# Kernel tuning notes

Measured on AMD Instinct MI355X. Metric: run time of the kernel, lower is better.

Reference implementation:

```python
import jax, jax.numpy as jnp
import numpy as np

N, E, V, H, HEADS, L, B = 20000, 320000, 100, 128, 3, 2, 200
NEG = 0.2   # leaky_relu negative_slope
EPS = 1e-5  # LayerNorm eps


def _mean_nodes(x, gid):
    # dgl.mean_nodes: per-graph mean of node features
    s = jax.ops.segment_sum(x, gid, num_segments=B)
    c = jax.ops.segment_sum(jnp.ones((x.shape[0], 1), x.dtype), gid, num_segments=B)
    return s / jnp.maximum(c, 1.0)


def _gat_layer(h, src, dst, Wn, bn, att, Ws, b, gamma, beta):
    # weight_node: Linear(H, H*HEADS)
    wv = (h @ Wn + bn).reshape(-1, HEADS, H)
    u = wv[src]  # [E, heads, H] gathered src features
    # attn = leaky_relu(sum(cat(u, v) * w_att)) split into u/v halves (no concat materialized)
    attn = (jnp.einsum('ehd,hd->eh', u, att[:, :H])
            + jnp.einsum('ehd,hd->eh', wv[dst], att[:, H:]))
    attn = jax.nn.leaky_relu(attn, NEG)  # [E, heads]
    # segment softmax over incoming edges of each dst node (mailbox softmax)
    m = jax.ops.segment_max(attn, dst, num_segments=N)
    m = jnp.where(jnp.isfinite(m), m, 0.0)
    e = jnp.exp(attn - m[dst])
    s = jax.ops.segment_sum(e, dst, num_segments=N)
    score = e / s[dst]
    agg = jax.ops.segment_sum(score[:, :, None] * u, dst, num_segments=N)  # [N, heads, H]
    res = agg.reshape(-1, HEADS * H) @ Ws + b
    # DGL leaves zero-in-degree nodes with zero reduced features (reduce_func never runs)
    has_in = jax.ops.segment_sum(jnp.ones((E,), h.dtype), dst, num_segments=N) > 0
    res = jnp.where(has_in[:, None], res, 0.0)
    x = res + h  # residual, then LayerNorm, relu (dropout is eval-mode identity)
    mu = jnp.mean(x, -1, keepdims=True)
    var = jnp.var(x, -1, keepdims=True)
    x = (x - mu) * jax.lax.rsqrt(var + EPS) * gamma + beta
    return jax.nn.relu(x)


def _gru_dir(x, Wih, Whh, bih, bhh, reverse):
    # torch nn.GRU single direction; x: [B, T, in]
    def step(hprev, xt):
        gi = xt @ Wih.T + bih
        gh = hprev @ Whh.T + bhh
        ir, iz, inn = jnp.split(gi, 3, -1)
        hr, hz, hn = jnp.split(gh, 3, -1)
        r = jax.nn.sigmoid(ir + hr)
        z = jax.nn.sigmoid(iz + hz)
        n = jnp.tanh(inn + r * hn)
        hnew = (1.0 - z) * n + z * hprev
        return hnew, hnew
    h0 = jnp.zeros((x.shape[0], Whh.shape[1]), x.dtype)
    hT, ys = jax.lax.scan(step, h0, jnp.swapaxes(x, 0, 1), reverse=reverse)
    return jnp.swapaxes(ys, 0, 1), hT


def setup_inputs() -> dict:
    key = jax.random.key(0)
    k = jax.random.split(key, 16)
    sc = 0.05
    return {
        'h': jax.random.normal(k[0], (N, H), jnp.float32),
        'wid': jax.random.randint(k[1], (N,), 0, V),
        'src': jax.random.randint(k[2], (E,), 0, N),
        'dst': jax.random.randint(k[3], (E,), 0, N),
        'graph_ids': jnp.sort(jax.random.randint(k[4], (N,), 0, B)),
        'proj_W': jax.random.normal(k[5], (V + H, H), jnp.float32) * sc,
        'proj_b': jnp.zeros((H,), jnp.float32),
        'conv_Wn': jax.random.normal(k[6], (L, H, HEADS * H), jnp.float32) * sc,
        'conv_bn': jnp.zeros((L, HEADS * H), jnp.float32),
        'conv_att': jax.random.normal(k[7], (L, HEADS, 2 * H), jnp.float32) * sc,
        'conv_Ws': jax.random.normal(k[8], (L, HEADS * H, H), jnp.float32) * sc,
        'conv_b': jnp.zeros((L, H), jnp.float32),
        'conv_gamma': jnp.ones((L, H), jnp.float32),
        'conv_beta': jnp.zeros((L, H), jnp.float32),
        'gru_Wih0': jax.random.normal(k[9], (2, 3 * H, H), jnp.float32) * sc,
        'gru_Whh0': jax.random.normal(k[10], (2, 3 * H, H), jnp.float32) * sc,
        'gru_bih0': jnp.zeros((2, 3 * H), jnp.float32),
        'gru_bhh0': jnp.zeros((2, 3 * H), jnp.float32),
        'gru_Wih1': jax.random.normal(k[11], (2, 3 * H, 2 * H), jnp.float32) * sc,
        'gru_Whh1': jax.random.normal(k[12], (2, 3 * H, H), jnp.float32) * sc,
        'gru_bih1': jnp.zeros((2, 3 * H), jnp.float32),
        'gru_bhh1': jnp.zeros((2, 3 * H), jnp.float32),
    }


def reference(h, wid, src, dst, graph_ids, proj_W, proj_b, conv_Wn, conv_bn, conv_att, conv_Ws, conv_b, conv_gamma, conv_beta, gru_Wih0, gru_Whh0, gru_bih0, gru_bhh0, gru_Wih1, gru_Whh1, gru_bih1, gru_bhh1):
    one_hot = jax.nn.one_hot(wid, V, dtype=h.dtype)
    hcur = jnp.concatenate([one_hot, h], -1) @ proj_W + proj_b  # project
    readouts = [_mean_nodes(hcur, graph_ids)]
    for l in range(L):
        hcur = _gat_layer(hcur, src, dst, conv_Wn[l], conv_bn[l], conv_att[l],
                          conv_Ws[l], conv_b[l], conv_gamma[l], conv_beta[l])
        readouts.append(_mean_nodes(hcur, graph_ids))
    x = jnp.stack(readouts, 1)  # [B, L+1, H] GRU readout sequence
    finals = []
    for (Wih, Whh, bih, bhh) in ((gru_Wih0, gru_Whh0, gru_bih0, gru_bhh0),
                                 (gru_Wih1, gru_Whh1, gru_bih1, gru_bhh1)):
        yf, hf = _gru_dir(x, Wih[0], Whh[0], bih[0], bhh[0], False)
        yb, hb = _gru_dir(x, Wih[1], Whh[1], bih[1], bhh[1], True)
        x = jnp.concatenate([yf, yb], -1)
        finals += [hf, hb]
    # torch returns h_n [num_layers*2, B, H]; module takes mean over dim 0
    return jnp.mean(jnp.stack(finals, 0), 0)  # [B, H]
```

## Files before the change

kernel.cpp:

```cpp
#include <hip/hip_runtime.h>
#include <cstddef>
#include <cstdint>

static constexpr int Nn    = 20000;
static constexpr int Ee    = 320000;
static constexpr int Vv    = 100;
static constexpr int Hh    = 128;
static constexpr int HEADS = 3;
static constexpr int Bb    = 200;
static constexpr float NEG = 0.2f;
static constexpr float EPS = 1e-5f;

typedef short bf16x8 __attribute__((ext_vector_type(8)));
typedef float f32x4  __attribute__((ext_vector_type(4)));

__device__ inline unsigned short bf16_rne(float x) {
    unsigned u = __builtin_bit_cast(unsigned, x);
    u += 0x7FFFu + ((u >> 16) & 1u);
    return (unsigned short)(u >> 16);
}
__device__ inline float bf16_f(unsigned short h) {
    unsigned u = ((unsigned)h) << 16;
    return __builtin_bit_cast(float, u);
}
__device__ inline float bf_lo(unsigned u) { return __builtin_bit_cast(float, u << 16); }
__device__ inline float bf_hi(unsigned u) { return __builtin_bit_cast(float, u & 0xFFFF0000u); }
__device__ inline float lrelu(float a) { return a >= 0.f ? a : NEG * a; }
__device__ inline float sigmoidf(float x) { return 1.f / (1.f + __expf(-x)); }

__global__ __launch_bounds__(1024) void scan_offsets(const int* __restrict__ deg,
                                                     int* __restrict__ offs,
                                                     int* __restrict__ cur) {
    __shared__ int sums[1024];
    const int tid = threadIdx.x;
    const int per = (Nn + 1023) >> 10;
    int begin = tid * per;
    int end = begin + per; if (end > Nn) end = Nn;
    if (begin > Nn) begin = Nn;
    int s = 0;
    for (int i = begin; i < end; i++) s += deg[i];
    sums[tid] = s;
    __syncthreads();
    for (int off = 1; off < 1024; off <<= 1) {
        int v = (tid >= off) ? sums[tid - off] : 0;
        __syncthreads();
        sums[tid] += v;
        __syncthreads();
    }
    int run = sums[tid] - s;
    for (int i = begin; i < end; i++) {
        offs[i] = run; cur[i] = run;
        run += deg[i];
    }
    if (end == Nn) offs[Nn] = run;
}

__global__ void fill_csr(const int* __restrict__ dst, const int* __restrict__ src,
                         int* __restrict__ cur, int* __restrict__ csrc) {
    for (int i = blockIdx.x * blockDim.x + threadIdx.x; i < Ee; i += gridDim.x * blockDim.x) {
        int p = atomicAdd(&cur[dst[i]], 1);
        csrc[p] = src[i];
    }
}

struct PrepArgs {
    const float *projW, *convWn, *convWs, *convAtt, *convBn, *convB;
    const float *Wih0, *Whh0, *Wih1, *Whh1;
    const int *gid, *dst;
    unsigned short *pBth, *pBtl;
    unsigned short *WfTh0, *WfTl0, *WfTh1, *WfTl1;
    float *vavd, *vc, *biasF;
    float *WihT0, *WhhT0, *WihT1, *WhhT1;
    int *goffs, *deg;
};

__device__ inline void wsplit(const float* B, int K, int N, int idx,
                              unsigned short* Bth, unsigned short* Btl) {
    int k = idx / N, n = idx - k * N;
    float v = B[idx];
    unsigned short h = bf16_rne(v);
    unsigned short l = bf16_rne(v - bf16_f(h));
    Bth[(size_t)n * K + k] = h;
    Btl[(size_t)n * K + k] = l;
}
__device__ inline void gruT(const float* W, int K, int idx, float* WT) {
    int d = idx / (384 * K);
    int r = idx - d * 384 * K;
    int j = r / K, k = r - j * K;
    WT[(size_t)d * K * 384 + (size_t)k * 384 + j] = W[idx];
}

__global__ void prep_all(PrepArgs a) {
    int i = blockIdx.x * blockDim.x + threadIdx.x;
    if (i < 16384) { wsplit(a.projW, 128, 128, i, a.pBth, a.pBtl); return; } i -= 16384;
#pragma unroll
    for (int l = 0; l < 2; l++) {
        if (i < 49152) {
            int k = i >> 7, c = i & 127;
            int h = k >> 7, i_ = k & 127;
            const float* wn = a.convWn + (size_t)l * 49152 + (size_t)i_ * 384 + h * 128;
            const float* ws = a.convWs + (size_t)l * 49152 + (size_t)(h * 128) * 128 + c;
            float v = 0.f;
            for (int j = 0; j < 128; j++) v += wn[j] * ws[(size_t)j * 128];
            unsigned short hi = bf16_rne(v);
            unsigned short lo = bf16_rne(v - bf16_f(hi));
            unsigned short* th = l ? a.WfTh1 : a.WfTh0;
            unsigned short* tl = l ? a.WfTl1 : a.WfTl0;
            th[(size_t)c * 384 + k] = hi;
            tl[(size_t)c * 384 + k] = lo;
            return;
        }
        i -= 49152;
    }
    if (i < 1536) {
        int l = i / 768, r = i % 768;
        int sd = r / 384, rr = r % 384, h = rr >> 7, i_ = rr & 127;
        const float* wn = a.convWn + (size_t)l * 49152 + (size_t)i_ * 384 + h * 128;
        const float* at = a.convAtt + l * 768 + h * 256 + sd * 128;
        float v = 0.f;
        for (int j = 0; j < 128; j++) v += wn[j] * at[j];
        a.vavd[i] = v;
        return;
    } i -= 1536;
    if (i < 12) {
        int l = i / 6, r = i % 6, sd = r / 3, h = r % 3;
        const float* bn = a.convBn + l * 384 + h * 128;
        const float* at = a.convAtt + l * 768 + h * 256 + sd * 128;
        float v = 0.f;
        for (int j = 0; j < 128; j++) v += bn[j] * at[j];
        a.vc[i] = v;
        return;
    } i -= 12;
    if (i < 256) {
        int l = i >> 7, c = i & 127;
        const float* bn = a.convBn + l * 384;
        const float* ws = a.convWs + (size_t)l * 49152 + c;
        float v = a.convB[l * 128 + c];
        for (int k = 0; k < 384; k++) v += bn[k] * ws[(size_t)k * 128];
        a.biasF[i] = v;
        return;
    } i -= 256;
    if (i < 98304)  { gruT(a.Wih0, 128, i, a.WihT0); return; }  i -= 98304;
    if (i < 98304)  { gruT(a.Whh0, 128, i, a.WhhT0); return; }  i -= 98304;
    if (i < 196608) { gruT(a.Wih1, 256, i, a.WihT1); return; }  i -= 196608;
    if (i < 98304)  { gruT(a.Whh1, 128, i, a.WhhT1); return; }  i -= 98304;
    if (i < Nn) {
        int g = a.gid[i];
        if (i == 0) { for (int b = 0; b <= g; b++) a.goffs[b] = 0; }
        else { int pg = a.gid[i - 1]; for (int b = pg + 1; b <= g; b++) a.goffs[b] = i; }
        if (i == Nn - 1) { for (int b = g + 1; b <= Bb; b++) a.goffs[b] = Nn; }
        return;
    } i -= Nn;
    if (i < Ee) atomicAdd(&a.deg[a.dst[i]], 1);
}

struct GArgs {
    const float* A; const unsigned short* Bth; const unsigned short* Btl;
    const float* bias; int M, K;
    const int* wid; const float* projW;
    const int* deg; const float* gamma; const float* beta;
    float* hcur;
    const int* gid; float* reado;
    const float* vavd; const float* vc;
    float* adf; float* addf;
    unsigned short* hb;
};

template <int MODE>
__global__ __launch_bounds__(256) void gemm_fused(GArgs a) {
    __shared__ unsigned short As_hi[32][40];
    __shared__ unsigned short As_lo[32][40];
    __shared__ unsigned short Bs_hi[128][40];
    __shared__ unsigned short Bs_lo[128][40];
    __shared__ float ytile[32][132];
    __shared__ float sred[6][32][4];
    __shared__ int sgid[32];
    const int tid  = threadIdx.x;
    const int row0 = blockIdx.y * 32;
    const int wn   = tid >> 6;
    const int L    = tid & 63;
    const int lrow = L & 15;
    const int lq   = L >> 4;
    const int K = a.K;

    f32x4 acc[2][2];
#pragma unroll
    for (int i = 0; i < 2; i++)
#pragma unroll
        for (int j = 0; j < 2; j++) acc[i][j] = (f32x4){0.f, 0.f, 0.f, 0.f};

    for (int kb = 0; kb < K; kb += 32) {
        {
            int m  = tid >> 3;
            int kq = (tid & 7) * 4;
            float4 v = *(const float4*)(a.A + (size_t)(row0 + m) * K + kb + kq);
            unsigned short h0 = bf16_rne(v.x), h1 = bf16_rne(v.y),
                           h2 = bf16_rne(v.z), h3 = bf16_rne(v.w);
            *(short4*)&As_hi[m][kq] = make_short4((short)h0, (short)h1, (short)h2, (short)h3);
            *(short4*)&As_lo[m][kq] = make_short4((short)bf16_rne(v.x - bf16_f(h0)),
                                                  (short)bf16_rne(v.y - bf16_f(h1)),
                                                  (short)bf16_rne(v.z - bf16_f(h2)),
                                                  (short)bf16_rne(v.w - bf16_f(h3)));
        }
        {
            int n  = tid >> 1;
            int kh = (tid & 1) * 16;
            const unsigned short* sh = a.Bth + (size_t)n * K + kb + kh;
            const unsigned short* sl = a.Btl + (size_t)n * K + kb + kh;
            *(float4*)&Bs_hi[n][kh]     = *(const float4*)sh;
            *(float4*)&Bs_hi[n][kh + 8] = *(const float4*)(sh + 8);
            *(float4*)&Bs_lo[n][kh]     = *(const float4*)sl;
            *(float4*)&Bs_lo[n][kh + 8] = *(const float4*)(sl + 8);
        }
        __syncthreads();
        bf16x8 ah[2], al[2], bh[2], bl[2];
#pragma unroll
        for (int mi = 0; mi < 2; mi++) {
            int r = mi * 16 + lrow;
            ah[mi] = *(const bf16x8*)&As_hi[r][lq * 8];
            al[mi] = *(const bf16x8*)&As_lo[r][lq * 8];
        }
#pragma unroll
        for (int ni = 0; ni < 2; ni++) {
            int r = wn * 32 + ni * 16 + lrow;
            bh[ni] = *(const bf16x8*)&Bs_hi[r][lq * 8];
            bl[ni] = *(const bf16x8*)&Bs_lo[r][lq * 8];
        }
#pragma unroll
        for (int mi = 0; mi < 2; mi++)
#pragma unroll
            for (int ni = 0; ni < 2; ni++) {
                acc[mi][ni] = __builtin_amdgcn_mfma_f32_16x16x32_bf16(ah[mi], bh[ni], acc[mi][ni], 0, 0, 0);
                acc[mi][ni] = __builtin_amdgcn_mfma_f32_16x16x32_bf16(ah[mi], bl[ni], acc[mi][ni], 0, 0, 0);
                acc[mi][ni] = __builtin_amdgcn_mfma_f32_16x16x32_bf16(al[mi], bh[ni], acc[mi][ni], 0, 0, 0);
            }
        __syncthreads();
    }

#pragma unroll
    for (int ni = 0; ni < 2; ni++) {
        float bb = a.bias[wn * 32 + ni * 16 + lrow];
#pragma unroll
        for (int mi = 0; mi < 2; mi++)
#pragma unroll
            for (int r = 0; r < 4; r++) acc[mi][ni][r] += bb;
    }

    if constexpr (MODE == 0) {
#pragma unroll
        for (int mi = 0; mi < 2; mi++)
#pragma unroll
            for (int r = 0; r < 4; r++) {
                int lr = mi * 16 + lq * 4 + r;
                int row = row0 + lr;
                int wi = a.wid[row];
#pragma unroll
                for (int ni = 0; ni < 2; ni++) {
                    int c = wn * 32 + ni * 16 + lrow;
                    float y = acc[mi][ni][r] + a.projW[(size_t)wi * 128 + c];
                    acc[mi][ni][r] = y;
                    a.hcur[(size_t)row * 128 + c] = y;
                    ytile[lr][c] = y;
                }
            }
    }

    if constexpr (MODE == 2) {
        __shared__ float red1[32][4], red2[32][4];
        float g4[2], be4[2];
#pragma unroll
        for (int ni = 0; ni < 2; ni++) {
            int c = wn * 32 + ni * 16 + lrow;
            g4[ni] = a.gamma[c]; be4[ni] = a.beta[c];
        }
#pragma unroll
        for (int mi = 0; mi < 2; mi++)
#pragma unroll
            for (int r = 0; r < 4; r++) {
                int lr = mi * 16 + lq * 4 + r;
                int row = row0 + lr;
                int dg = a.deg[row];
#pragma unroll
                for (int ni = 0; ni < 2; ni++) {
                    int c = wn * 32 + ni * 16 + lrow;
                    float hold = a.hcur[(size_t)row * 128 + c];
                    acc[mi][ni][r] = hold + (dg > 0 ? acc[mi][ni][r] : 0.f);
                }
            }
#pragma unroll
        for (int mi = 0; mi < 2; mi++)
#pragma unroll
            for (int r = 0; r < 4; r++) {
                float ps = acc[mi][0][r] + acc[mi][1][r];
#pragma unroll
                for (int o = 1; o < 16; o <<= 1) ps += __shfl_xor(ps, o, 64);
                if (lrow == 0) red1[mi * 16 + lq * 4 + r][wn] = ps;
            }
        __syncthreads();
#pragma unroll
        for (int mi = 0; mi < 2; mi++)
#pragma unroll
            for (int r = 0; r < 4; r++) {
                int lr = mi * 16 + lq * 4 + r;
                float mu = (red1[lr][0] + red1[lr][1] + red1[lr][2] + red1[lr][3]) * (1.f / 128.f);
                float qs = 0.f;
#pragma unroll
                for (int ni = 0; ni < 2; ni++) {
                    float dx = acc[mi][ni][r] - mu;
                    qs += dx * dx;
                }
#pragma unroll
                for (int o = 1; o < 16; o <<= 1) qs += __shfl_xor(qs, o, 64);
                if (lrow == 0) red2[lr][wn] = qs;
            }
        __syncthreads();
#pragma unroll
        for (int mi = 0; mi < 2; mi++)
#pragma unroll
            for (int r = 0; r < 4; r++) {
                int lr = mi * 16 + lq * 4 + r;
                int row = row0 + lr;
                float mu = (red1[lr][0] + red1[lr][1] + red1[lr][2] + red1[lr][3]) * (1.f / 128.f);
                float var = (red2[lr][0] + red2[lr][1] + red2[lr][2] + red2[lr][3]) * (1.f / 128.f);
                float rs = rsqrtf(var + EPS);
#pragma unroll
                for (int ni = 0; ni < 2; ni++) {
                    int c = wn * 32 + ni * 16 + lrow;
                    float y = fmaxf((acc[mi][ni][r] - mu) * rs * g4[ni] + be4[ni], 0.f);
                    acc[mi][ni][r] = y;
                    a.hcur[(size_t)row * 128 + c] = y;
                    ytile[lr][c] = y;
                }
            }
    }

    if (tid < 32) sgid[tid] = a.gid[row0 + tid];

    const bool dots = (a.vavd != nullptr);
    if (dots) {
        float vv0[6], vv1[6];
#pragma unroll
        for (int d = 0; d < 6; d++) {
            vv0[d] = a.vavd[d * 128 + wn * 32 + lrow];
            vv1[d] = a.vavd[d * 128 + wn * 32 + 16 + lrow];
        }
#pragma unroll
        for (int d = 0; d < 6; d++) {
#pragma unroll
            for (int mi = 0; mi < 2; mi++)
#pragma unroll
                for (int r = 0; r < 4; r++) {
                    float ps = acc[mi][0][r] * vv0[d] + acc[mi][1][r] * vv1[d];
#pragma unroll
                    for (int o = 1; o < 16; o <<= 1) ps += __shfl_xor(ps, o, 64);
                    if (lrow == 0) sred[d][mi * 16 + lq * 4 + r][wn] = ps;
                }
        }
    }
    __syncthreads();

    {
        int j = tid & 127, hh = tid >> 7;
        float sum = 0.f; int curg = -1;
        for (int r = hh * 16; r < hh * 16 + 16; r++) {
            int g = sgid[r];
            if (g != curg) {
                if (curg >= 0) atomicAdd(&a.reado[(size_t)curg * 128 + j], sum);
                sum = 0.f; curg = g;
            }
            sum += ytile[r][j];
        }
        if (curg >= 0) atomicAdd(&a.reado[(size_t)curg * 128 + j], sum);
    }

    if (dots) {
        if (tid < 192) {
            int row = tid & 31, d = tid >> 5;
            float s = sred[d][row][0] + sred[d][row][1] + sred[d][row][2] + sred[d][row][3]
                    + a.vc[d];
            int node = row0 + row;
            int sd = d / 3, h = d - sd * 3;
            float* dstp = sd ? a.addf : a.adf;
            dstp[(size_t)node * 4 + h] = s;
        }
        {
            int row = tid >> 3, c0 = (tid & 7) * 16;
            unsigned* dst = (unsigned*)(a.hb + (size_t)(row0 + row) * 128 + c0);
#pragma unroll
            for (int q = 0; q < 8; q++) {
                unsigned lo = bf16_rne(ytile[row][c0 + 2 * q]);
                unsigned hi = bf16_rne(ytile[row][c0 + 2 * q + 1]);
                dst[q] = lo | (hi << 16);
            }
        }
    }
}

__global__ __launch_bounds__(256) void gat_gather(const unsigned short* __restrict__ hb,
                                                  const float4* __restrict__ ad,
                                                  const float4* __restrict__ add,
                                                  const int* __restrict__ offs,
                                                  const int* __restrict__ csrc,
                                                  float* __restrict__ T) {
    __shared__ float4 slot[4][64];
    const int n = (blockIdx.x * 256 + threadIdx.x) >> 6;
    const int wv_ = threadIdx.x >> 6;
    const int L = threadIdx.x & 63;
    if (n >= Nn) return;
    const int start = offs[n];
    const int deg = offs[n + 1] - start;
    float2* o2 = (float2*)(T + (size_t)n * 384);
    if (deg == 0) {
        float2 z = make_float2(0.f, 0.f);
        o2[L] = z; o2[64 + L] = z; o2[128 + L] = z;
        return;
    }
    const float4 adn = add[n];
    float2 t0 = make_float2(0.f, 0.f), t1 = t0, t2 = t0;

    if (deg <= 64) {
        int sn = 0; float e0 = 0.f, e1 = 0.f, e2 = 0.f;
        if (L < deg) {
            sn = csrc[start + L];
            float4 a4 = ad[sn];
            e0 = __expf(lrelu(a4.x + adn.x));
            e1 = __expf(lrelu(a4.y + adn.y));
            e2 = __expf(lrelu(a4.z + adn.z));
        }
        float s0 = e0, s1 = e1, s2 = e2;
#pragma unroll
        for (int o = 32; o > 0; o >>= 1) {
            s0 += __shfl_xor(s0, o, 64);
            s1 += __shfl_xor(s1, o, 64);
            s2 += __shfl_xor(s2, o, 64);
        }
        slot[wv_][L] = make_float4(__builtin_bit_cast(float, sn),
                                   e0 / s0, e1 / s1, e2 / s2);
        __builtin_amdgcn_wave_barrier();
#pragma unroll 2
        for (int j = 0; j < deg; j++) {
            float4 sc = slot[wv_][j];
            int s_n = __builtin_bit_cast(int, sc.x);
            unsigned u = ((const unsigned*)(hb + (size_t)s_n * 128))[L];
            float x0 = bf_lo(u), x1 = bf_hi(u);
            t0.x += sc.y * x0; t0.y += sc.y * x1;
            t1.x += sc.z * x0; t1.y += sc.z * x1;
            t2.x += sc.w * x0; t2.y += sc.w * x1;
        }
    } else {
        float s0 = 0.f, s1 = 0.f, s2 = 0.f;
        for (int i = L; i < deg; i += 64) {
            int sn = csrc[start + i];
            float4 a4 = ad[sn];
            s0 += __expf(lrelu(a4.x + adn.x));
            s1 += __expf(lrelu(a4.y + adn.y));
            s2 += __expf(lrelu(a4.z + adn.z));
        }
#pragma unroll
        for (int o = 32; o > 0; o >>= 1) {
            s0 += __shfl_xor(s0, o, 64);
            s1 += __shfl_xor(s1, o, 64);
            s2 += __shfl_xor(s2, o, 64);
        }
        float i0 = 1.f / s0, i1 = 1.f / s1, i2 = 1.f / s2;
        for (int base = 0; base < deg; base += 64) {
            int cnt = deg - base; if (cnt > 64) cnt = 64;
            if (L < cnt) {
                int sn = csrc[start + base + L];
                float4 a4 = ad[sn];
                slot[wv_][L] = make_float4(__builtin_bit_cast(float, sn),
                                           __expf(lrelu(a4.x + adn.x)) * i0,
                                           __expf(lrelu(a4.y + adn.y)) * i1,
                                           __expf(lrelu(a4.z + adn.z)) * i2);
            }
            __builtin_amdgcn_wave_barrier();
            for (int j = 0; j < cnt; j++) {
                float4 sc = slot[wv_][j];
                int s_n = __builtin_bit_cast(int, sc.x);
                unsigned u = ((const unsigned*)(hb + (size_t)s_n * 128))[L];
                float x0 = bf_lo(u), x1 = bf_hi(u);
                t0.x += sc.y * x0; t0.y += sc.y * x1;
                t1.x += sc.z * x0; t1.y += sc.z * x1;
                t2.x += sc.w * x0; t2.y += sc.w * x1;
            }
            __builtin_amdgcn_wave_barrier();
        }
    }
    o2[L] = t0; o2[64 + L] = t1; o2[128 + L] = t2;
}

static constexpr int GNB = 2;

__global__ __launch_bounds__(384, 2) void gru_l0(const float* __restrict__ reado,
                                                 const int* __restrict__ goffs,
                                                 const float* __restrict__ WihT0,
                                                 const float* __restrict__ WhhT0,
                                                 const float* __restrict__ bih0,
                                                 const float* __restrict__ bhh0,
                                                 float* __restrict__ y0g,
                                                 float* __restrict__ out) {
    const int dir = blockIdx.y;
    const int b0 = blockIdx.x * GNB;
    const int j = threadIdx.x;
    __shared__ float xs[3][128][GNB];
    __shared__ float hs[128][GNB];
    __shared__ float gis[384][GNB];
    __shared__ float ghs[384][GNB];
    __shared__ float invc_s[GNB];
    if (j < GNB) {
        int cnt = goffs[b0 + j + 1] - goffs[b0 + j];
        invc_s[j] = 1.f / fmaxf((float)cnt, 1.f);
    }
    if (j < 128) {
#pragma unroll
        for (int nb = 0; nb < GNB; nb++) hs[j][nb] = 0.f;
    }
    __syncthreads();
    for (int i = j; i < 3 * 128 * GNB; i += 384) {
        int nb = i % GNB, k = (i / GNB) & 127, t = i / (128 * GNB);
        xs[t][k][nb] = reado[(size_t)t * Bb * Hh + (size_t)(b0 + nb) * Hh + k] * invc_s[nb];
    }
    __syncthreads();

    const float* Wi = WihT0 + (size_t)dir * 128 * 384;
    const float* Wh = WhhT0 + (size_t)dir * 128 * 384;
    const float bij = bih0[dir * 384 + j];
    const float bhj = bhh0[dir * 384 + j];
    int tmap[3];
    tmap[0] = dir ? 2 : 0; tmap[1] = 1; tmap[2] = dir ? 0 : 2;

    float gi[3][GNB];
#pragma unroll
    for (int s = 0; s < 3; s++)
#pragma unroll
        for (int nb = 0; nb < GNB; nb++) gi[s][nb] = bij;
    for (int k = 0; k < 128; k++) {
        float w = Wi[(size_t)k * 384 + j];
#pragma unroll
        for (int s = 0; s < 3; s++)
#pragma unroll
            for (int nb = 0; nb < GNB; nb++)
                gi[s][nb] += w * xs[tmap[s]][k][nb];
    }

    float wh[128];
#pragma unroll
    for (int k = 0; k < 128; k++) wh[k] = Wh[(size_t)k * 384 + j];

#pragma unroll
    for (int step = 0; step < 3; step++) {
        float g[GNB];
#pragma unroll
        for (int nb = 0; nb < GNB; nb++) g[nb] = bhj;
#pragma unroll
        for (int k = 0; k < 128; k++) {
#pragma unroll
            for (int nb = 0; nb < GNB; nb++) g[nb] += wh[k] * hs[k][nb];
        }
#pragma unroll
        for (int nb = 0; nb < GNB; nb++) {
            ghs[j][nb] = g[nb];
            gis[j][nb] = gi[step][nb];
        }
        __syncthreads();
        if (j < 128) {
            const int t = tmap[step];
#pragma unroll
            for (int nb = 0; nb < GNB; nb++) {
                float r  = sigmoidf(gis[j][nb] + ghs[j][nb]);
                float z  = sigmoidf(gis[j + 128][nb] + ghs[j + 128][nb]);
                float nn = tanhf(gis[j + 256][nb] + r * ghs[j + 256][nb]);
                float hnew = (1.f - z) * nn + z * hs[j][nb];
                hs[j][nb] = hnew;
                y0g[((size_t)t * Bb + (b0 + nb)) * 256 + dir * 128 + j] = hnew;
                if (step == 2)
                    atomicAdd(&out[(size_t)(b0 + nb) * Hh + j], 0.25f * hnew);
            }
        }
        __syncthreads();
    }
}

__global__ __launch_bounds__(384, 2) void gru_l1(const float* __restrict__ y0g,
                                                 const float* __restrict__ WihT1,
                                                 const float* __restrict__ WhhT1,
                                                 const float* __restrict__ bih1,
                                                 const float* __restrict__ bhh1,
                                                 float* __restrict__ out) {
    const int dir = blockIdx.y;
    const int b0 = blockIdx.x * GNB;
    const int j = threadIdx.x;
    __shared__ float ys[3][256][GNB];
    __shared__ float hs[128][GNB];
    __shared__ float gis[384][GNB];
    __shared__ float ghs[384][GNB];
    if (j < 128) {
#pragma unroll
        for (int nb = 0; nb < GNB; nb++) hs[j][nb] = 0.f;
    }
    for (int i = j; i < 3 * 256 * GNB; i += 384) {
        int nb = i % GNB, u = (i / GNB) & 255, t = i / (256 * GNB);
        ys[t][u][nb] = y0g[((size_t)t * Bb + (b0 + nb)) * 256 + u];
    }
    __syncthreads();

    const float* Wi = WihT1 + (size_t)dir * 256 * 384;
    const float* Wh = WhhT1 + (size_t)dir * 128 * 384;
    const float bij = bih1[dir * 384 + j];
    const float bhj = bhh1[dir * 384 + j];
    int tmap[3];
    tmap[0] = dir ? 2 : 0; tmap[1] = 1; tmap[2] = dir ? 0 : 2;

    float gi[3][GNB];
#pragma unroll
    for (int s = 0; s < 3; s++)
#pragma unroll
        for (int nb = 0; nb < GNB; nb++) gi[s][nb] = bij;
    for (int k = 0; k < 256; k++) {
        float w = Wi[(size_t)k * 384 + j];
#pragma unroll
        for (int s = 0; s < 3; s++)
#pragma unroll
            for (int nb = 0; nb < GNB; nb++)
                gi[s][nb] += w * ys[tmap[s]][k][nb];
    }

    float wh[128];
#pragma unroll
    for (int k = 0; k < 128; k++) wh[k] = Wh[(size_t)k * 384 + j];

#pragma unroll
    for (int step = 0; step < 3; step++) {
        float g[GNB];
#pragma unroll
        for (int nb = 0; nb < GNB; nb++) g[nb] = bhj;
#pragma unroll
        for (int k = 0; k < 128; k++) {
#pragma unroll
            for (int nb = 0; nb < GNB; nb++) g[nb] += wh[k] * hs[k][nb];
        }
#pragma unroll
        for (int nb = 0; nb < GNB; nb++) {
            ghs[j][nb] = g[nb];
            gis[j][nb] = gi[step][nb];
        }
        __syncthreads();
        if (j < 128) {
#pragma unroll
            for (int nb = 0; nb < GNB; nb++) {
                float r  = sigmoidf(gis[j][nb] + ghs[j][nb]);
                float z  = sigmoidf(gis[j + 128][nb] + ghs[j + 128][nb]);
                float nn = tanhf(gis[j + 256][nb] + r * ghs[j + 256][nb]);
                float hnew = (1.f - z) * nn + z * hs[j][nb];
                hs[j][nb] = hnew;
                if (step == 2)
                    atomicAdd(&out[(size_t)(b0 + nb) * Hh + j], 0.25f * hnew);
            }
        }
        __syncthreads();
    }
}

extern "C" void kernel_launch(void* const* d_in, const int* in_sizes, int n_in,
                              void* d_out, int out_size, void* d_ws, size_t ws_size,
                              hipStream_t stream) {
    const float* h      = (const float*)d_in[0];
    const int*   wid    = (const int*)d_in[1];
    const int*   src    = (const int*)d_in[2];
    const int*   dst    = (const int*)d_in[3];
    const int*   gid    = (const int*)d_in[4];
    const float* projW  = (const float*)d_in[5];
    const float* projB  = (const float*)d_in[6];
    const float* convWn = (const float*)d_in[7];
    const float* convBn = (const float*)d_in[8];
    const float* convAtt= (const float*)d_in[9];
    const float* convWs = (const float*)d_in[10];
    const float* convB  = (const float*)d_in[11];
    const float* convG  = (const float*)d_in[12];
    const float* convBe = (const float*)d_in[13];
    const float* Wih0   = (const float*)d_in[14];
    const float* Whh0   = (const float*)d_in[15];
    const float* bih0   = (const float*)d_in[16];
    const float* bhh0   = (const float*)d_in[17];
    const float* Wih1   = (const float*)d_in[18];
    const float* Whh1   = (const float*)d_in[19];
    const float* bih1   = (const float*)d_in[20];
    const float* bhh1   = (const float*)d_in[21];
    float* out = (float*)d_out;

    char* p = (char*)d_ws;
    auto align16 = [&]() { p = (char*)(((uintptr_t)p + 15) & ~(uintptr_t)15); };
    auto alloc_f = [&](size_t n) { align16(); float* r = (float*)p; p += n * sizeof(float); return r; };
    auto alloc_i = [&](size_t n) { align16(); int* r = (int*)p; p += n * sizeof(int); return r; };
    auto alloc_s = [&](size_t n) { align16(); unsigned short* r = (unsigned short*)p; p += n * sizeof(unsigned short); return r; };
    float* hcur  = alloc_f((size_t)Nn * 128);
    float* T     = alloc_f((size_t)Nn * 384);
    float* adbuf = alloc_f((size_t)Nn * 4);
    float* addbuf= alloc_f((size_t)Nn * 4);
    float* reado = alloc_f((size_t)3 * Bb * Hh);
    int* deg  = alloc_i(Nn);
    const size_t zero_bytes = (size_t)3 * Bb * Hh * sizeof(float) + Nn * sizeof(int);
    float* WihT0 = alloc_f((size_t)2 * 128 * 384);
    float* WhhT0 = alloc_f((size_t)2 * 128 * 384);
    float* WihT1 = alloc_f((size_t)2 * 256 * 384);
    float* WhhT1 = alloc_f((size_t)2 * 128 * 384);
    float* vavd  = alloc_f(1536);
    float* vc    = alloc_f(12);
    float* biasF = alloc_f(256);
    float* y0g   = alloc_f((size_t)3 * Bb * 256);
    int* offs = alloc_i(Nn + 1);
    int* cur  = alloc_i(Nn);
    int* csrc = alloc_i(Ee);
    int* goffs = alloc_i(Bb + 1);
    unsigned short* hb = alloc_s((size_t)Nn * 128);
    unsigned short* pBth = alloc_s(128 * 128);
    unsigned short* pBtl = alloc_s(128 * 128);
    unsigned short* WfTh[2] = { alloc_s(128 * 384), alloc_s(128 * 384) };
    unsigned short* WfTl[2] = { alloc_s(128 * 384), alloc_s(128 * 384) };

    hipMemsetAsync(reado, 0, zero_bytes, stream);
    hipMemsetAsync(out, 0, (size_t)Bb * Hh * sizeof(float), stream);

    PrepArgs pa;
    pa.projW = projW + (size_t)Vv * Hh;
    pa.convWn = convWn; pa.convWs = convWs; pa.convAtt = convAtt;
    pa.convBn = convBn; pa.convB = convB;
    pa.Wih0 = Wih0; pa.Whh0 = Whh0; pa.Wih1 = Wih1; pa.Whh1 = Whh1;
    pa.gid = gid; pa.dst = dst;
    pa.pBth = pBth; pa.pBtl = pBtl;
    pa.WfTh0 = WfTh[0]; pa.WfTl0 = WfTl[0]; pa.WfTh1 = WfTh[1]; pa.WfTl1 = WfTl[1];
    pa.vavd = vavd; pa.vc = vc; pa.biasF = biasF;
    pa.WihT0 = WihT0; pa.WhhT0 = WhhT0; pa.WihT1 = WihT1; pa.WhhT1 = WhhT1;
    pa.goffs = goffs; pa.deg = deg;
    const int prep_total = 16384 + 2 * 49152 + 1536 + 12 + 256 + 98304 + 98304 + 196608 + 98304 + Nn + Ee;
    prep_all<<<(prep_total + 255) / 256, 256, 0, stream>>>(pa);

    scan_offsets<<<1, 1024, 0, stream>>>(deg, offs, cur);
    fill_csr<<<1250, 256, 0, stream>>>(dst, src, cur, csrc);

    {
        GArgs g = {};
        g.A = h; g.Bth = pBth; g.Btl = pBtl; g.bias = projB;
        g.M = Nn; g.K = 128;
        g.wid = wid; g.projW = projW; g.hcur = hcur;
        g.gid = gid; g.reado = reado;
        g.vavd = vavd; g.vc = vc; g.adf = adbuf; g.addf = addbuf; g.hb = hb;
        gemm_fused<0><<<dim3(1, Nn / 32), 256, 0, stream>>>(g);
    }

    const int nwaveblocks = (Nn * 64 + 255) / 256;
    for (int l = 0; l < 2; l++) {
        gat_gather<<<nwaveblocks, 256, 0, stream>>>(hb, (const float4*)adbuf, (const float4*)addbuf,
                                                    offs, csrc, T);
        {
            GArgs g = {};
            g.A = T; g.Bth = WfTh[l]; g.Btl = WfTl[l]; g.bias = biasF + l * 128;
            g.M = Nn; g.K = 384;
            g.deg = deg; g.gamma = convG + l * Hh; g.beta = convBe + l * Hh;
            g.hcur = hcur;
            g.gid = gid; g.reado = reado + (size_t)(l + 1) * Bb * Hh;
            if (l == 0) { g.vavd = vavd + 768; g.vc = vc + 6; g.adf = adbuf; g.addf = addbuf; g.hb = hb; }
            gemm_fused<2><<<dim3(1, Nn / 32), 256, 0, stream>>>(g);
        }
    }

    gru_l0<<<dim3(Bb / GNB, 2), 384, 0, stream>>>(reado, goffs, WihT0, WhhT0, bih0, bhh0,
                                                  y0g, out);
    gru_l1<<<dim3(Bb / GNB, 2), 384, 0, stream>>>(y0g, WihT1, WhhT1, bih1, bhh1, out);
}
```

Measured before the change: 397.5 us.

## Restructure GRU kernels to stream weights and broadcast hidden state via shuffles

Both GRU kernels stop holding all 128 recurrent weights in registers. They now reload Whh from global memory each step and broadcast the hidden state across the wavefront with __shfl instead of reading shared-memory arrays. The input projection reads readout and layer-0 outputs directly from global memory as float4 and is unrolled by 4, and the first step skips the recurrent matmul because the hidden state starts at zero. This cuts register pressure and shared-memory staging in exchange for repeated global weight loads, but these tiny kernels are a small part of the total GAT pipeline.

```diff
diff --git a/kernel.cpp b/kernel.cpp
--- a/kernel.cpp
+++ b/kernel.cpp
@@ -489,175 +489,187 @@
     o2[L] = t0; o2[64 + L] = t1; o2[128 + L] = t2;
 }
 
-static constexpr int GNB = 2;
-
-__global__ __launch_bounds__(384, 2) void gru_l0(const float* __restrict__ reado,
-                                                 const int* __restrict__ goffs,
-                                                 const float* __restrict__ WihT0,
-                                                 const float* __restrict__ WhhT0,
-                                                 const float* __restrict__ bih0,
-                                                 const float* __restrict__ bhh0,
-                                                 float* __restrict__ y0g,
-                                                 float* __restrict__ out) {
+__global__ __launch_bounds__(384) void gru_l0(const float* __restrict__ reado,
+                                              const int* __restrict__ goffs,
+                                              const float* __restrict__ WihT0,
+                                              const float* __restrict__ WhhT0,
+                                              const float* __restrict__ bih0,
+                                              const float* __restrict__ bhh0,
+                                              float* __restrict__ y0g,
+                                              float* __restrict__ out) {
     const int dir = blockIdx.y;
-    const int b0 = blockIdx.x * GNB;
+    const int b0 = blockIdx.x * 2;
     const int j = threadIdx.x;
-    __shared__ float xs[3][128][GNB];
-    __shared__ float hs[128][GNB];
-    __shared__ float gis[384][GNB];
-    __shared__ float ghs[384][GNB];
-    __shared__ float invc_s[GNB];
-    if (j < GNB) {
-        int cnt = goffs[b0 + j + 1] - goffs[b0 + j];
-        invc_s[j] = 1.f / fmaxf((float)cnt, 1.f);
-    }
-    if (j < 128) {
-#pragma unroll
-        for (int nb = 0; nb < GNB; nb++) hs[j][nb] = 0.f;
-    }
-    __syncthreads();
-    for (int i = j; i < 3 * 128 * GNB; i += 384) {
-        int nb = i % GNB, k = (i / GNB) & 127, t = i / (128 * GNB);
-        xs[t][k][nb] = reado[(size_t)t * Bb * Hh + (size_t)(b0 + nb) * Hh + k] * invc_s[nb];
-    }
-    __syncthreads();
+    const int L = j & 63;
+    __shared__ float gis[384][2];
+    __shared__ float ghs[384][2];
+    __shared__ float hsh[128][2];
+
+    float invc[2];
+#pragma unroll
+    for (int nb = 0; nb < 2; nb++) {
+        int cnt = goffs[b0 + nb + 1] - goffs[b0 + nb];
+        invc[nb] = 1.f / fmaxf((float)cnt, 1.f);
+    }
 
     const float* Wi = WihT0 + (size_t)dir * 128 * 384;
     const float* Wh = WhhT0 + (size_t)dir * 128 * 384;
     const float bij = bih0[dir * 384 + j];
     const float bhj = bhh0[dir * 384 + j];
-    int tmap[3];
-    tmap[0] = dir ? 2 : 0; tmap[1] = 1; tmap[2] = dir ? 0 : 2;
-
-    float gi[3][GNB];
-#pragma unroll
-    for (int s = 0; s < 3; s++)
-#pragma unroll
-        for (int nb = 0; nb < GNB; nb++) gi[s][nb] = bij;
-    for (int k = 0; k < 128; k++) {
-        float w = Wi[(size_t)k * 384 + j];
-#pragma unroll
-        for (int s = 0; s < 3; s++)
-#pragma unroll
-            for (int nb = 0; nb < GNB; nb++)
-                gi[s][nb] += w * xs[tmap[s]][k][nb];
-    }
-
-    float wh[128];
-#pragma unroll
-    for (int k = 0; k < 128; k++) wh[k] = Wh[(size_t)k * 384 + j];
-
+
+    float gi[3][2];
+#pragma unroll
+    for (int t = 0; t < 3; t++) { gi[t][0] = 0.f; gi[t][1] = 0.f; }
+#pragma unroll 4
+    for (int k = 0; k < 128; k += 4) {
+        float w0 = Wi[(size_t)(k + 0) * 384 + j];
+        float w1 = Wi[(size_t)(k + 1) * 384 + j];
+        float w2 = Wi[(size_t)(k + 2) * 384 + j];
+        float w3 = Wi[(size_t)(k + 3) * 384 + j];
+#pragma unroll
+        for (int t = 0; t < 3; t++)
+#pragma unroll
+            for (int nb = 0; nb < 2; nb++) {
+                float4 x = *(const float4*)(reado + ((size_t)t * Bb + b0 + nb) * 128 + k);
+                gi[t][nb] += w0 * x.x + w1 * x.y + w2 * x.z + w3 * x.w;
+            }
+    }
+#pragma unroll
+    for (int t = 0; t < 3; t++)
+#pragma unroll
+        for (int nb = 0; nb < 2; nb++)
+            gi[t][nb] = gi[t][nb] * invc[nb] + bij;
+
+    float h0[2] = {0.f, 0.f};
+    float h1[2] = {0.f, 0.f};
 #pragma unroll
     for (int step = 0; step < 3; step++) {
-        float g[GNB];
-#pragma unroll
-        for (int nb = 0; nb < GNB; nb++) g[nb] = bhj;
-#pragma unroll
-        for (int k = 0; k < 128; k++) {
-#pragma unroll
-            for (int nb = 0; nb < GNB; nb++) g[nb] += wh[k] * hs[k][nb];
-        }
-#pragma unroll
-        for (int nb = 0; nb < GNB; nb++) {
-            ghs[j][nb] = g[nb];
-            gis[j][nb] = gi[step][nb];
-        }
+        float g0 = bhj, g1 = bhj;
+        if (step > 0) {
+#pragma unroll
+            for (int k = 0; k < 64; k++) {
+                float w = Wh[(size_t)k * 384 + j];
+                g0 += w * __shfl(h0[0], k, 64);
+                g1 += w * __shfl(h0[1], k, 64);
+            }
+#pragma unroll
+            for (int k = 0; k < 64; k++) {
+                float w = Wh[(size_t)(64 + k) * 384 + j];
+                g0 += w * __shfl(h1[0], k, 64);
+                g1 += w * __shfl(h1[1], k, 64);
+            }
+        }
+        float gs0 = dir ? gi[2 - step][0] : gi[step][0];
+        float gs1 = dir ? gi[2 - step][1] : gi[step][1];
+        *(float2*)&gis[j][0] = make_float2(gs0, gs1);
+        *(float2*)&ghs[j][0] = make_float2(g0, g1);
         __syncthreads();
         if (j < 128) {
-            const int t = tmap[step];
-#pragma unroll
-            for (int nb = 0; nb < GNB; nb++) {
+            const int t = dir ? 2 - step : step;
+#pragma unroll
+            for (int nb = 0; nb < 2; nb++) {
                 float r  = sigmoidf(gis[j][nb] + ghs[j][nb]);
                 float z  = sigmoidf(gis[j + 128][nb] + ghs[j + 128][nb]);
                 float nn = tanhf(gis[j + 256][nb] + r * ghs[j + 256][nb]);
-                float hnew = (1.f - z) * nn + z * hs[j][nb];
-                hs[j][nb] = hnew;
+                float hprev = (step == 0) ? 0.f : hsh[j][nb];
+                float hnew = (1.f - z) * nn + z * hprev;
+                hsh[j][nb] = hnew;
                 y0g[((size_t)t * Bb + (b0 + nb)) * 256 + dir * 128 + j] = hnew;
                 if (step == 2)
                     atomicAdd(&out[(size_t)(b0 + nb) * Hh + j], 0.25f * hnew);
             }
         }
         __syncthreads();
-    }
-}
-
-__global__ __launch_bounds__(384, 2) void gru_l1(const float* __restrict__ y0g,
-                                                 const float* __restrict__ WihT1,
-                                                 const float* __restrict__ WhhT1,
-                                                 const float* __restrict__ bih1,
-                                                 const float* __restrict__ bhh1,
-                                                 float* __restrict__ out) {
+        if (step < 2) {
+            float2 a = *(const float2*)&hsh[L][0];
+            float2 b = *(const float2*)&hsh[64 + L][0];
+            h0[0] = a.x; h0[1] = a.y;
+            h1[0] = b.x; h1[1] = b.y;
+        }
+    }
+}
+
+__global__ __launch_bounds__(384) void gru_l1(const float* __restrict__ y0g,
+                                              const float* __restrict__ WihT1,
+                                              const float* __restrict__ WhhT1,
+                                              const float* __restrict__ bih1,
+                                              const float* __restrict__ bhh1,
+                                              float* __restrict__ out) {
     const int dir = blockIdx.y;
-    const int b0 = blockIdx.x * GNB;
+    const int b0 = blockIdx.x * 2;
     const int j = threadIdx.x;
-    __shared__ float ys[3][256][GNB];
-    __shared__ float hs[128][GNB];
-    __shared__ float gis[384][GNB];
-    __shared__ float ghs[384][GNB];
-    if (j < 128) {
-#pragma unroll
-        for (int nb = 0; nb < GNB; nb++) hs[j][nb] = 0.f;
-    }
-    for (int i = j; i < 3 * 256 * GNB; i += 384) {
-        int nb = i % GNB, u = (i / GNB) & 255, t = i / (256 * GNB);
-        ys[t][u][nb] = y0g[((size_t)t * Bb + (b0 + nb)) * 256 + u];
-    }
-    __syncthreads();
+    const int L = j & 63;
+    __shared__ float gis[384][2];
+    __shared__ float ghs[384][2];
+    __shared__ float hsh[128][2];
 
     const float* Wi = WihT1 + (size_t)dir * 256 * 384;
     const float* Wh = WhhT1 + (size_t)dir * 128 * 384;
     const float bij = bih1[dir * 384 + j];
     const float bhj = bhh1[dir * 384 + j];
-    int tmap[3];
-    tmap[0] = dir ? 2 : 0; tmap[1] = 1; tmap[2] = dir ? 0 : 2;
-
-    float gi[3][GNB];
-#pragma unroll
-    for (int s = 0; s < 3; s++)
-#pragma unroll
-        for (int nb = 0; nb < GNB; nb++) gi[s][nb] = bij;
-    for (int k = 0; k < 256; k++) {
-        float w = Wi[(size_t)k * 384 + j];
-#pragma unroll
-        for (int s = 0; s < 3; s++)
-#pragma unroll
-            for (int nb = 0; nb < GNB; nb++)
-                gi[s][nb] += w * ys[tmap[s]][k][nb];
-    }
-
-    float wh[128];
-#pragma unroll
-    for (int k = 0; k < 128; k++) wh[k] = Wh[(size_t)k * 384 + j];
-
+
+    float gi[3][2];
+#pragma unroll
+    for (int t = 0; t < 3; t++) { gi[t][0] = bij; gi[t][1] = bij; }
+#pragma unroll 4
+    for (int k = 0; k < 256; k += 4) {
+        float w0 = Wi[(size_t)(k + 0) * 384 + j];
+        float w1 = Wi[(size_t)(k + 1) * 384 + j];
+        float w2 = Wi[(size_t)(k + 2) * 384 + j];
+        float w3 = Wi[(size_t)(k + 3) * 384 + j];
+#pragma unroll
+        for (int t = 0; t < 3; t++)
+#pragma unroll
+            for (int nb = 0; nb < 2; nb++) {
+                float4 x = *(const float4*)(y0g + ((size_t)t * Bb + b0 + nb) * 256 + k);
+                gi[t][nb] += w0 * x.x + w1 * x.y + w2 * x.z + w3 * x.w;
+            }
+    }
+
+    float h0[2] = {0.f, 0.f};
+    float h1[2] = {0.f, 0.f};
 #pragma unroll
     for (int step = 0; step < 3; step++) {
-        float g[GNB];
-#pragma unroll
-        for (int nb = 0; nb < GNB; nb++) g[nb] = bhj;
-#pragma unroll
-        for (int k = 0; k < 128; k++) {
-#pragma unroll
-            for (int nb = 0; nb < GNB; nb++) g[nb] += wh[k] * hs[k][nb];
-        }
-#pragma unroll
-        for (int nb = 0; nb < GNB; nb++) {
-            ghs[j][nb] = g[nb];
-            gis[j][nb] = gi[step][nb];
-        }
+        float g0 = bhj, g1 = bhj;
+        if (step > 0) {
+#pragma unroll
+            for (int k = 0; k < 64; k++) {
+                float w = Wh[(size_t)k * 384 + j];
+                g0 += w * __shfl(h0[0], k, 64);
+                g1 += w * __shfl(h0[1], k, 64);
+            }
+#pragma unroll
+            for (int k = 0; k < 64; k++) {
+                float w = Wh[(size_t)(64 + k) * 384 + j];
+                g0 += w * __shfl(h1[0], k, 64);
+                g1 += w * __shfl(h1[1], k, 64);
+            }
+        }
+        float gs0 = dir ? gi[2 - step][0] : gi[step][0];
+        float gs1 = dir ? gi[2 - step][1] : gi[step][1];
+        *(float2*)&gis[j][0] = make_float2(gs0, gs1);
+        *(float2*)&ghs[j][0] = make_float2(g0, g1);
         __syncthreads();
         if (j < 128) {
 #pragma unroll
-            for (int nb = 0; nb < GNB; nb++) {
+            for (int nb = 0; nb < 2; nb++) {
                 float r  = sigmoidf(gis[j][nb] + ghs[j][nb]);
                 float z  = sigmoidf(gis[j + 128][nb] + ghs[j + 128][nb]);
                 float nn = tanhf(gis[j + 256][nb] + r * ghs[j + 256][nb]);
-                float hnew = (1.f - z) * nn + z * hs[j][nb];
-                hs[j][nb] = hnew;
+                float hprev = (step == 0) ? 0.f : hsh[j][nb];
+                float hnew = (1.f - z) * nn + z * hprev;
+                hsh[j][nb] = hnew;
                 if (step == 2)
                     atomicAdd(&out[(size_t)(b0 + nb) * Hh + j], 0.25f * hnew);
             }
         }
         __syncthreads();
+        if (step < 2) {
+            float2 a = *(const float2*)&hsh[L][0];
+            float2 b = *(const float2*)&hsh[64 + L][0];
+            h0[0] = a.x; h0[1] = a.y;
+            h1[0] = b.x; h1[1] = b.y;
+        }
     }
 }
 
@@ -764,7 +776,7 @@
         }
     }
 
-    gru_l0<<<dim3(Bb / GNB, 2), 384, 0, stream>>>(reado, goffs, WihT0, WhhT0, bih0, bhh0,
-                                                  y0g, out);
-    gru_l1<<<dim3(Bb / GNB, 2), 384, 0, stream>>>(y0g, WihT1, WhhT1, bih1, bhh1, out);
-}
+    gru_l0<<<dim3(Bb / 2, 2), 384, 0, stream>>>(reado, goffs, WihT0, WhhT0, bih0, bhh0,
+                                                y0g, out);
+    gru_l1<<<dim3(Bb / 2, 2), 384, 0, stream>>>(y0g, WihT1, WhhT1, bih1, bhh1, out);
+}
```

Result: slower. 586.7 us (+47.6%).
